# Kernel optimization log

Hardware: AMD Instinct MI355X
Metric: run time of the kernel (lower is better)

## Reference

```python
import jax, jax.numpy as jnp
import numpy as np

EPS = 1e-12  # tf.math.l2_normalize epsilon

def _l2n(x, axis):
    # faithful to K.l2_normalize: x / sqrt(max(sum(x^2), eps))
    return x / jnp.sqrt(jnp.maximum(jnp.sum(x * x, axis=axis, keepdims=True), EPS))

def setup_inputs() -> dict:
    key = jax.random.key(0)
    k1, k2, k3 = jax.random.split(key, 3)
    B, T, D, P = 32, 1024, 256, 20
    inp_a = jax.random.normal(k1, (B, T, D), dtype=jnp.float32)
    inp_b = jax.random.normal(k2, (B, T, D), dtype=jnp.float32)
    # 'uniform' keras initializer -> U(-0.05, 0.05)
    W = jax.random.uniform(k3, (P, D), dtype=jnp.float32, minval=-0.05, maxval=0.05)
    return {"inp_a": inp_a, "inp_b": inp_b, "W": W}

def reference(inp_a, inp_b, W):
    # inp_a, inp_b: (B, T, D); W: (P, D)
    oa = _l2n(inp_a, -1)
    ob = _l2n(inp_b, -1)
    # K.batch_dot(ob, oa, axes=[1,1]) -> (B, D, D), contract over seq
    alpha = jnp.einsum('btd,bte->bde', ob, oa)
    alpha = _l2n(alpha, 1)
    # K.batch_dot(ob, alpha, axes=[2,1]) -> (B, T, D)
    hmean = jnp.einsum('btd,bde->bte', ob, alpha)
    # Per perspective i the original computes the (T,T) batch_dot of
    # l2norm(hmean*W_i) and l2norm(inp_a*W_i), then masks with eye(T) and sums
    # -> the diagonal, i.e. per-token cosine similarity. Since both vectors are
    # scaled by the same W_i, cos = <a*h, W_i^2> / (||a*W_i|| * ||h*W_i||),
    # computed directly in linear cost for all perspectives at once.
    W2 = W * W  # (P, D)
    num = jnp.einsum('btd,pd->btp', inp_a * hmean, W2)
    sa = jnp.einsum('btd,pd->btp', inp_a * inp_a, W2)
    sh = jnp.einsum('btd,pd->btp', hmean * hmean, W2)
    persp = num / (jnp.sqrt(jnp.maximum(sa, EPS)) * jnp.sqrt(jnp.maximum(sh, EPS)))
    return (persp, persp)
```

## Files before the change

### kernel.cpp

```cpp
#include <hip/hip_runtime.h>
#include <math.h>

#define BB 32
#define TT 1024
#define DD 256
#define PP 20
constexpr float EPS = 1e-12f;

typedef __attribute__((ext_vector_type(8))) short bf16x8;
typedef __attribute__((ext_vector_type(4))) float f32x4;

static __device__ __forceinline__ unsigned short f2bf(float f) {
    union { float f; unsigned int u; } c; c.f = f;
    const unsigned int u = c.u;
    return (unsigned short)((u + 0x7FFFu + ((u >> 16) & 1u)) >> 16);
}

__global__ __launch_bounds__(256) void k_prep(const float* __restrict__ in,
                                              unsigned short* __restrict__ outT,
                                              unsigned short* __restrict__ outN) {
    __shared__ unsigned short Tls[DD][66];
    const int b = blockIdx.y;
    const int t0 = blockIdx.x * 64;
    const int wave = threadIdx.x >> 6;
    const int lane = threadIdx.x & 63;
    const float* src = in + (size_t)b * TT * DD;
    for (int pass = 0; pass < 16; ++pass) {
        const int tl = pass * 4 + wave;
        const int t = t0 + tl;
        const float4 v =
            *reinterpret_cast<const float4*>(&src[(size_t)t * DD + lane * 4]);
        float ss = v.x * v.x + v.y * v.y + v.z * v.z + v.w * v.w;
#pragma unroll
        for (int off = 32; off; off >>= 1) ss += __shfl_xor(ss, off);
        const float sc = 1.0f / sqrtf(fmaxf(ss, EPS));
        Tls[lane * 4 + 0][tl] = f2bf(v.x * sc);
        Tls[lane * 4 + 1][tl] = f2bf(v.y * sc);
        Tls[lane * 4 + 2][tl] = f2bf(v.z * sc);
        Tls[lane * 4 + 3][tl] = f2bf(v.w * sc);
        if (outN) {
            ushort4 r;
            r.x = f2bf(v.x); r.y = f2bf(v.y); r.z = f2bf(v.z); r.w = f2bf(v.w);
            *reinterpret_cast<ushort4*>(&outN[((size_t)b * TT + t) * DD + lane * 4]) = r;
        }
    }
    __syncthreads();
    const int d = threadIdx.x;
    unsigned short* dst = outT + ((size_t)b * DD + d) * TT + t0;
#pragma unroll
    for (int k = 0; k < 8; ++k) {
        unsigned short tmp[8];
#pragma unroll
        for (int j = 0; j < 8; ++j) tmp[j] = Tls[d][k * 8 + j];
        *reinterpret_cast<uint4*>(&dst[k * 8]) = *reinterpret_cast<const uint4*>(tmp);
    }
}

template <int M, int N, int K>
__global__ __launch_bounds__(256) void k_gemm(const unsigned short* __restrict__ A,
                                              const unsigned short* __restrict__ B,
                                              float* __restrict__ C) {
    __shared__ unsigned short As[2][64][40];
    __shared__ unsigned short Bs[2][64][40];
    const int tid = threadIdx.x;
    const int b = blockIdx.y;
    constexpr int NTILES = N / 64;
    const int m0 = (blockIdx.x / NTILES) * 64;
    const int n0 = (blockIdx.x % NTILES) * 64;
    const unsigned short* pA = A + (size_t)b * M * K + (size_t)m0 * K;
    const unsigned short* pB = B + (size_t)b * N * K + (size_t)n0 * K;
    const int srow = tid >> 2;
    const int skoff = (tid & 3) * 8;
    const int wave = tid >> 6;
    const int lane = tid & 63;
    const int wm = (wave >> 1) * 32;
    const int wn = (wave & 1) * 32;
    const int fr = lane & 15;
    const int fc = lane >> 4;
    f32x4 acc[2][2] = {};
    uint4 ra, rb;

    ra = *reinterpret_cast<const uint4*>(&pA[(size_t)srow * K + skoff]);
    rb = *reinterpret_cast<const uint4*>(&pB[(size_t)srow * K + skoff]);
    *reinterpret_cast<uint4*>(&As[0][srow][skoff]) = ra;
    *reinterpret_cast<uint4*>(&Bs[0][srow][skoff]) = rb;

    constexpr int NT = K / 32;
    for (int t = 0; t < NT; ++t) {
        if (t + 1 < NT) {
            const int k0 = (t + 1) * 32;
            ra = *reinterpret_cast<const uint4*>(&pA[(size_t)srow * K + k0 + skoff]);
            rb = *reinterpret_cast<const uint4*>(&pB[(size_t)srow * K + k0 + skoff]);
        }
        __syncthreads();
        const int cur = t & 1;
        bf16x8 af[2], bfr[2];
#pragma unroll
        for (int i = 0; i < 2; ++i) {
            af[i]  = *reinterpret_cast<const bf16x8*>(&As[cur][wm + i * 16 + fr][fc * 8]);
            bfr[i] = *reinterpret_cast<const bf16x8*>(&Bs[cur][wn + i * 16 + fr][fc * 8]);
        }
#pragma unroll
        for (int i = 0; i < 2; ++i)
#pragma unroll
            for (int j = 0; j < 2; ++j)
                acc[i][j] = __builtin_amdgcn_mfma_f32_16x16x32_bf16(af[i], bfr[j],
                                                                    acc[i][j], 0, 0, 0);
        if (t + 1 < NT) {
            const int nxt = (t + 1) & 1;
            *reinterpret_cast<uint4*>(&As[nxt][srow][skoff]) = ra;
            *reinterpret_cast<uint4*>(&Bs[nxt][srow][skoff]) = rb;
        }
    }
    float* pC = C + (size_t)b * M * N;
#pragma unroll
    for (int i = 0; i < 2; ++i)
#pragma unroll
        for (int j = 0; j < 2; ++j) {
            const int rbase = m0 + wm + i * 16 + fc * 4;
            const int col = n0 + wn + j * 16 + fr;
#pragma unroll
            for (int r = 0; r < 4; ++r)
                pC[(size_t)(rbase + r) * N + col] = acc[i][j][r];
        }
}

__global__ __launch_bounds__(256) void k_alphanorm2(const float* __restrict__ src,
                                                    unsigned short* __restrict__ dst) {
    const int wave = threadIdx.x >> 6;
    const int lane = threadIdx.x & 63;
    const size_t row = (size_t)blockIdx.x * 4 + wave;
    const float4 v = reinterpret_cast<const float4*>(src + row * DD)[lane];
    float s = v.x * v.x + v.y * v.y + v.z * v.z + v.w * v.w;
#pragma unroll
    for (int off = 32; off; off >>= 1) s += __shfl_xor(s, off);
    const float sc = 1.0f / sqrtf(fmaxf(s, EPS));
    ushort4 r;
    r.x = f2bf(v.x * sc); r.y = f2bf(v.y * sc);
    r.z = f2bf(v.z * sc); r.w = f2bf(v.w * sc);
    reinterpret_cast<ushort4*>(dst + row * DD)[lane] = r;
}

__global__ __launch_bounds__(256) void k_persp(const float* __restrict__ inp_a,
                                               const float* __restrict__ hmean,
                                               const float* __restrict__ W,
                                               float* __restrict__ out) {
    __shared__ float w2L[PP * DD];
    for (int i = threadIdx.x; i < PP * DD; i += 256) {
        const float w = W[i];
        w2L[i] = w * w;
    }
    __syncthreads();
    const int wave = threadIdx.x >> 6;
    const int lane = threadIdx.x & 63;
    const int q = lane & 7;
    const int r = lane >> 3;
    const size_t row = (size_t)blockIdx.x * 32 + wave * 8 + r;
    const float* pa = inp_a + row * DD + q * 4;
    const float* ph = hmean + row * DD + q * 4;

    float acc[PP][3] = {};
#pragma unroll
    for (int quad = 0; quad < 8; ++quad) {
        const float4 a4 = *reinterpret_cast<const float4*>(pa + quad * 32);
        const float4 h4 = *reinterpret_cast<const float4*>(ph + quad * 32);
        const float ah[4] = {a4.x * h4.x, a4.y * h4.y, a4.z * h4.z, a4.w * h4.w};
        const float aa[4] = {a4.x * a4.x, a4.y * a4.y, a4.z * a4.z, a4.w * a4.w};
        const float hh[4] = {h4.x * h4.x, h4.y * h4.y, h4.z * h4.z, h4.w * h4.w};
#pragma unroll
        for (int p = 0; p < PP; ++p) {
            const float4 w4 =
                *reinterpret_cast<const float4*>(&w2L[p * DD + quad * 32 + q * 4]);
            const float wv[4] = {w4.x, w4.y, w4.z, w4.w};
#pragma unroll
            for (int j = 0; j < 4; ++j) {
                acc[p][0] += ah[j] * wv[j];
                acc[p][1] += aa[j] * wv[j];
                acc[p][2] += hh[j] * wv[j];
            }
        }
    }
#pragma unroll
    for (int p = 0; p < PP; ++p)
#pragma unroll
        for (int s = 0; s < 3; ++s) {
            float v = acc[p][s];
            v += __shfl_xor(v, 1);
            v += __shfl_xor(v, 2);
            v += __shfl_xor(v, 4);
            acc[p][s] = v;
        }
    if (q == 0) {
        float res[PP];
#pragma unroll
        for (int p = 0; p < PP; ++p) {
            const float sa = sqrtf(fmaxf(acc[p][1], EPS));
            const float sh = sqrtf(fmaxf(acc[p][2], EPS));
            res[p] = acc[p][0] / (sa * sh);
        }
        float* o1 = out + row * PP;
        float* o2 = o1 + (size_t)BB * TT * PP;
#pragma unroll
        for (int k = 0; k < 5; ++k) {
            const float4 v = reinterpret_cast<const float4*>(res)[k];
            reinterpret_cast<float4*>(o1)[k] = v;
            reinterpret_cast<float4*>(o2)[k] = v;
        }
    }
}

extern "C" void kernel_launch(void* const* d_in, const int* in_sizes, int n_in,
                              void* d_out, int out_size, void* d_ws, size_t ws_size,
                              hipStream_t stream) {
    const float* inp_a = (const float*)d_in[0];
    const float* inp_b = (const float*)d_in[1];
    const float* W = (const float*)d_in[2];
    float* out = (float*)d_out;

    unsigned short* oaT = (unsigned short*)d_ws;
    unsigned short* obT = oaT + (size_t)BB * DD * TT;
    float* hmean = (float*)d_ws;
    unsigned short* bnat = obT + (size_t)BB * DD * TT;
    float* alphaT = (float*)(bnat + (size_t)BB * TT * DD);
    unsigned short* alphaTb = (unsigned short*)(alphaT + (size_t)BB * DD * DD);

    k_prep<<<dim3(TT / 64, BB), 256, 0, stream>>>(inp_a, oaT, nullptr);
    k_prep<<<dim3(TT / 64, BB), 256, 0, stream>>>(inp_b, obT, bnat);
    k_gemm<DD, DD, TT><<<dim3(16, BB), 256, 0, stream>>>(oaT, obT, alphaT);
    k_alphanorm2<<<BB * DD / 4, 256, 0, stream>>>(alphaT, alphaTb);
    k_gemm<TT, DD, DD><<<dim3(64, BB), 256, 0, stream>>>(bnat, alphaTb, hmean);
    k_persp<<<BB * TT / 32, 256, 0, stream>>>(inp_a, hmean, W, out);
}
```

Measured before the change: 203.2 us.

## Split-K the alpha GEMM and move perspective reductions onto bf16 MFMA

The D×D alpha GEMM (K=1024) is split into two K-halves across a grid z dimension, writing partial sums that the normalisation kernel adds together. This raises block count from 512 to 1024 for better occupancy, at the cost of extra workspace traffic. The perspective kernel is rewritten to compute the three W²-weighted reductions as bf16 MFMA products against a packed W² tile in shared memory, replacing scalar FMAs and shuffle reductions. The bf16 rounding of a·h, a², h² and W² lowers precision of the cosine outputs.

```diff
diff --git a/kernel.cpp b/kernel.cpp
--- a/kernel.cpp
+++ b/kernel.cpp
@@ -56,7 +56,7 @@
     }
 }
 
-template <int M, int N, int K>
+template <int M, int N, int K, int KS>
 __global__ __launch_bounds__(256) void k_gemm(const unsigned short* __restrict__ A,
                                               const unsigned short* __restrict__ B,
                                               float* __restrict__ C) {
@@ -65,10 +65,12 @@
     const int tid = threadIdx.x;
     const int b = blockIdx.y;
     constexpr int NTILES = N / 64;
+    constexpr int KSL = K / KS;
     const int m0 = (blockIdx.x / NTILES) * 64;
     const int n0 = (blockIdx.x % NTILES) * 64;
-    const unsigned short* pA = A + (size_t)b * M * K + (size_t)m0 * K;
-    const unsigned short* pB = B + (size_t)b * N * K + (size_t)n0 * K;
+    const int kbeg = blockIdx.z * KSL;
+    const unsigned short* pA = A + (size_t)b * M * K + (size_t)m0 * K + kbeg;
+    const unsigned short* pB = B + (size_t)b * N * K + (size_t)n0 * K + kbeg;
     const int srow = tid >> 2;
     const int skoff = (tid & 3) * 8;
     const int wave = tid >> 6;
@@ -85,7 +87,7 @@
     *reinterpret_cast<uint4*>(&As[0][srow][skoff]) = ra;
     *reinterpret_cast<uint4*>(&Bs[0][srow][skoff]) = rb;
 
-    constexpr int NT = K / 32;
+    constexpr int NT = KSL / 32;
     for (int t = 0; t < NT; ++t) {
         if (t + 1 < NT) {
             const int k0 = (t + 1) * 32;
@@ -112,7 +114,7 @@
             *reinterpret_cast<uint4*>(&Bs[nxt][srow][skoff]) = rb;
         }
     }
-    float* pC = C + (size_t)b * M * N;
+    float* pC = C + (size_t)blockIdx.z * BB * M * N + (size_t)b * M * N;
 #pragma unroll
     for (int i = 0; i < 2; ++i)
 #pragma unroll
@@ -125,12 +127,17 @@
         }
 }
 
-__global__ __launch_bounds__(256) void k_alphanorm2(const float* __restrict__ src,
+__global__ __launch_bounds__(256) void k_alphanorm2(const float* __restrict__ p0,
+                                                    const float* __restrict__ p1,
                                                     unsigned short* __restrict__ dst) {
     const int wave = threadIdx.x >> 6;
     const int lane = threadIdx.x & 63;
     const size_t row = (size_t)blockIdx.x * 4 + wave;
-    const float4 v = reinterpret_cast<const float4*>(src + row * DD)[lane];
+    float4 v = reinterpret_cast<const float4*>(p0 + row * DD)[lane];
+    if (p1) {
+        const float4 w = reinterpret_cast<const float4*>(p1 + row * DD)[lane];
+        v.x += w.x; v.y += w.y; v.z += w.z; v.w += w.w;
+    }
     float s = v.x * v.x + v.y * v.y + v.z * v.z + v.w * v.w;
 #pragma unroll
     for (int off = 32; off; off >>= 1) s += __shfl_xor(s, off);
@@ -141,70 +148,96 @@
     reinterpret_cast<ushort4*>(dst + row * DD)[lane] = r;
 }
 
-__global__ __launch_bounds__(256) void k_persp(const float* __restrict__ inp_a,
-                                               const float* __restrict__ hmean,
-                                               const float* __restrict__ W,
-                                               float* __restrict__ out) {
-    __shared__ float w2L[PP * DD];
-    for (int i = threadIdx.x; i < PP * DD; i += 256) {
-        const float w = W[i];
-        w2L[i] = w * w;
+__global__ __launch_bounds__(256) void k_persp2(const float* __restrict__ inp_a,
+                                                const float* __restrict__ hmean,
+                                                const float* __restrict__ W,
+                                                float* __restrict__ out) {
+    __shared__ uint4 Bpk[8 * 2 * 64];
+    const int tid = threadIdx.x;
+#pragma unroll
+    for (int i = 0; i < 4; ++i) {
+        const int ne = tid + i * 256;
+        const int kstep = ne >> 7;
+        const int j = (ne >> 6) & 1;
+        const int ln = ne & 63;
+        const int p = j * 16 + (ln & 15);
+        const int k0 = kstep * 32 + (ln >> 4) * 8;
+        unsigned short w8[8];
+        if (p < PP) {
+#pragma unroll
+            for (int e = 0; e < 8; ++e) {
+                const float w = W[p * DD + k0 + e];
+                w8[e] = f2bf(w * w);
+            }
+        } else {
+#pragma unroll
+            for (int e = 0; e < 8; ++e) w8[e] = 0;
+        }
+        Bpk[ne] = *reinterpret_cast<const uint4*>(w8);
     }
     __syncthreads();
-    const int wave = threadIdx.x >> 6;
-    const int lane = threadIdx.x & 63;
-    const int q = lane & 7;
-    const int r = lane >> 3;
-    const size_t row = (size_t)blockIdx.x * 32 + wave * 8 + r;
-    const float* pa = inp_a + row * DD + q * 4;
-    const float* ph = hmean + row * DD + q * 4;
-
-    float acc[PP][3] = {};
-#pragma unroll
-    for (int quad = 0; quad < 8; ++quad) {
-        const float4 a4 = *reinterpret_cast<const float4*>(pa + quad * 32);
-        const float4 h4 = *reinterpret_cast<const float4*>(ph + quad * 32);
-        const float ah[4] = {a4.x * h4.x, a4.y * h4.y, a4.z * h4.z, a4.w * h4.w};
-        const float aa[4] = {a4.x * a4.x, a4.y * a4.y, a4.z * a4.z, a4.w * a4.w};
-        const float hh[4] = {h4.x * h4.x, h4.y * h4.y, h4.z * h4.z, h4.w * h4.w};
-#pragma unroll
-        for (int p = 0; p < PP; ++p) {
-            const float4 w4 =
-                *reinterpret_cast<const float4*>(&w2L[p * DD + quad * 32 + q * 4]);
-            const float wv[4] = {w4.x, w4.y, w4.z, w4.w};
-#pragma unroll
-            for (int j = 0; j < 4; ++j) {
-                acc[p][0] += ah[j] * wv[j];
-                acc[p][1] += aa[j] * wv[j];
-                acc[p][2] += hh[j] * wv[j];
+
+    const int wave = tid >> 6;
+    const int lane = tid & 63;
+    const int fr = lane & 15;
+    const int fc = lane >> 4;
+    const size_t row = (size_t)blockIdx.x * 64 + wave * 16 + fr;
+    const float* pa = inp_a + row * DD + fc * 8;
+    const float* ph = hmean + row * DD + fc * 8;
+    const bf16x8* bp = reinterpret_cast<const bf16x8*>(Bpk);
+
+    f32x4 acc[3][2] = {};
+    float4 a0 = *reinterpret_cast<const float4*>(pa);
+    float4 a1 = *reinterpret_cast<const float4*>(pa + 4);
+    float4 h0 = *reinterpret_cast<const float4*>(ph);
+    float4 h1 = *reinterpret_cast<const float4*>(ph + 4);
+
+    for (int t = 0; t < 8; ++t) {
+        float4 na0, na1, nh0, nh1;
+        if (t < 7) {
+            na0 = *reinterpret_cast<const float4*>(pa + (t + 1) * 32);
+            na1 = *reinterpret_cast<const float4*>(pa + (t + 1) * 32 + 4);
+            nh0 = *reinterpret_cast<const float4*>(ph + (t + 1) * 32);
+            nh1 = *reinterpret_cast<const float4*>(ph + (t + 1) * 32 + 4);
+        }
+        const float av[8] = {a0.x, a0.y, a0.z, a0.w, a1.x, a1.y, a1.z, a1.w};
+        const float hv[8] = {h0.x, h0.y, h0.z, h0.w, h1.x, h1.y, h1.z, h1.w};
+        unsigned short ah[8], aa[8], hh[8];
+#pragma unroll
+        for (int e = 0; e < 8; ++e) {
+            ah[e] = f2bf(av[e] * hv[e]);
+            aa[e] = f2bf(av[e] * av[e]);
+            hh[e] = f2bf(hv[e] * hv[e]);
+        }
+        const bf16x8 pf0 = *reinterpret_cast<const bf16x8*>(ah);
+        const bf16x8 pf1 = *reinterpret_cast<const bf16x8*>(aa);
+        const bf16x8 pf2 = *reinterpret_cast<const bf16x8*>(hh);
+        const bf16x8 bf0 = bp[(t * 2 + 0) * 64 + lane];
+        const bf16x8 bf1 = bp[(t * 2 + 1) * 64 + lane];
+        acc[0][0] = __builtin_amdgcn_mfma_f32_16x16x32_bf16(pf0, bf0, acc[0][0], 0, 0, 0);
+        acc[0][1] = __builtin_amdgcn_mfma_f32_16x16x32_bf16(pf0, bf1, acc[0][1], 0, 0, 0);
+        acc[1][0] = __builtin_amdgcn_mfma_f32_16x16x32_bf16(pf1, bf0, acc[1][0], 0, 0, 0);
+        acc[1][1] = __builtin_amdgcn_mfma_f32_16x16x32_bf16(pf1, bf1, acc[1][1], 0, 0, 0);
+        acc[2][0] = __builtin_amdgcn_mfma_f32_16x16x32_bf16(pf2, bf0, acc[2][0], 0, 0, 0);
+        acc[2][1] = __builtin_amdgcn_mfma_f32_16x16x32_bf16(pf2, bf1, acc[2][1], 0, 0, 0);
+        a0 = na0; a1 = na1; h0 = nh0; h1 = nh1;
+    }
+
+    const size_t rowbase = (size_t)blockIdx.x * 64 + wave * 16 + fc * 4;
+#pragma unroll
+    for (int j = 0; j < 2; ++j) {
+        const int p = j * 16 + fr;
+        if (p < PP) {
+#pragma unroll
+            for (int r = 0; r < 4; ++r) {
+                const float num = acc[0][j][r];
+                const float sa = sqrtf(fmaxf(acc[1][j][r], EPS));
+                const float sh = sqrtf(fmaxf(acc[2][j][r], EPS));
+                const float v = num / (sa * sh);
+                const size_t o = (rowbase + r) * PP + p;
+                out[o] = v;
+                out[(size_t)BB * TT * PP + o] = v;
             }
-        }
-    }
-#pragma unroll
-    for (int p = 0; p < PP; ++p)
-#pragma unroll
-        for (int s = 0; s < 3; ++s) {
-            float v = acc[p][s];
-            v += __shfl_xor(v, 1);
-            v += __shfl_xor(v, 2);
-            v += __shfl_xor(v, 4);
-            acc[p][s] = v;
-        }
-    if (q == 0) {
-        float res[PP];
-#pragma unroll
-        for (int p = 0; p < PP; ++p) {
-            const float sa = sqrtf(fmaxf(acc[p][1], EPS));
-            const float sh = sqrtf(fmaxf(acc[p][2], EPS));
-            res[p] = acc[p][0] / (sa * sh);
-        }
-        float* o1 = out + row * PP;
-        float* o2 = o1 + (size_t)BB * TT * PP;
-#pragma unroll
-        for (int k = 0; k < 5; ++k) {
-            const float4 v = reinterpret_cast<const float4*>(res)[k];
-            reinterpret_cast<float4*>(o1)[k] = v;
-            reinterpret_cast<float4*>(o2)[k] = v;
         }
     }
 }
@@ -217,17 +250,24 @@
     const float* W = (const float*)d_in[2];
     float* out = (float*)d_out;
 
+    const size_t NTD = (size_t)BB * TT * DD;
+    const size_t NDD = (size_t)BB * DD * DD;
     unsigned short* oaT = (unsigned short*)d_ws;
-    unsigned short* obT = oaT + (size_t)BB * DD * TT;
+    unsigned short* obT = oaT + NTD;
     float* hmean = (float*)d_ws;
-    unsigned short* bnat = obT + (size_t)BB * DD * TT;
-    float* alphaT = (float*)(bnat + (size_t)BB * TT * DD);
-    unsigned short* alphaTb = (unsigned short*)(alphaT + (size_t)BB * DD * DD);
+    unsigned short* bnat = obT + NTD;
+    float* aP0 = (float*)(bnat + NTD);
+    const bool SPLIT = ws_size >= (size_t)(NTD * 2 * 3 + NDD * 4 * 2 + NDD * 2);
+    float* aP1 = SPLIT ? aP0 + NDD : nullptr;
+    unsigned short* aTb = (unsigned short*)(aP0 + (SPLIT ? 2 * NDD : NDD));
 
     k_prep<<<dim3(TT / 64, BB), 256, 0, stream>>>(inp_a, oaT, nullptr);
     k_prep<<<dim3(TT / 64, BB), 256, 0, stream>>>(inp_b, obT, bnat);
-    k_gemm<DD, DD, TT><<<dim3(16, BB), 256, 0, stream>>>(oaT, obT, alphaT);
-    k_alphanorm2<<<BB * DD / 4, 256, 0, stream>>>(alphaT, alphaTb);
-    k_gemm<TT, DD, DD><<<dim3(64, BB), 256, 0, stream>>>(bnat, alphaTb, hmean);
-    k_persp<<<BB * TT / 32, 256, 0, stream>>>(inp_a, hmean, W, out);
-}
+    if (SPLIT)
+        k_gemm<DD, DD, TT, 2><<<dim3(16, BB, 2), 256, 0, stream>>>(oaT, obT, aP0);
+    else
+        k_gemm<DD, DD, TT, 1><<<dim3(16, BB, 1), 256, 0, stream>>>(oaT, obT, aP0);
+    k_alphanorm2<<<BB * DD / 4, 256, 0, stream>>>(aP0, aP1, aTb);
+    k_gemm<TT, DD, DD, 1><<<dim3(64, BB, 1), 256, 0, stream>>>(bnat, aTb, hmean);
+    k_persp2<<<BB * TT / 64, 256, 0, stream>>>(inp_a, hmean, W, out);
+}
```

After: 184.0 us. 9.4% less time.
